# Kernel tuning notes

Hardware: AMD Instinct MI355X
Metric: run time of the kernel (lower is better)

The kernel has to match this reference:

```python
import jax, jax.numpy as jnp
import numpy as np

DIM = 2048
N_HEADS = 16
HEAD_DIM = DIM // N_HEADS
MAX_SEQ_LEN = 2048
THRESHOLD = 0.7
LN_EPS = 1e-5


def _layernorm(x, g, b):
    mu = jnp.mean(x, axis=-1, keepdims=True)
    var = jnp.mean(jnp.square(x - mu), axis=-1, keepdims=True)
    return (x - mu) * jax.lax.rsqrt(var + LN_EPS) * g + b


def _act_quant(x):
    # 8-bit absmax activation quantization (per-tensor), straight-through
    s = 127.0 / jnp.maximum(jnp.max(jnp.abs(x)), 1e-5)
    xq = jnp.clip(jnp.round(x * s), -128.0, 127.0) / s
    return x + jax.lax.stop_gradient(xq - x)


def _ternary_quant(w):
    # W1.58 ternary: zero weights below threshold*mean|w|, scale = mean |w| over survivors
    delta = THRESHOLD * jnp.mean(jnp.abs(w))
    mask = (jnp.abs(w) > delta).astype(w.dtype)
    alpha = jnp.sum(jnp.abs(w) * mask) / jnp.maximum(jnp.sum(mask), 1.0)
    wq = jnp.sign(w) * mask * alpha
    return w + jax.lax.stop_gradient(wq - w)


def _bitlinear(x, w, g, b):
    x = _layernorm(x, g, b)
    xq = _act_quant(x)
    wq = _ternary_quant(w)
    return xq @ wq.T


def _rope_tables():
    inv = 1.0 / (10000.0 ** (np.arange(0, HEAD_DIM, 2, dtype=np.float32) / HEAD_DIM))
    t = np.arange(MAX_SEQ_LEN, dtype=np.float32)
    ang = np.outer(t, inv)  # (max_seq, head_dim/2)
    return jnp.asarray(np.cos(ang)), jnp.asarray(np.sin(ang))


def _apply_rope(x, cos_t, sin_t):
    # Faithful to source: x is (B, H, S, D) and freqs are indexed by x.shape[1] == H
    n = x.shape[1]
    xr = x.reshape(*x.shape[:-1], HEAD_DIM // 2, 2)
    a, b = xr[..., 0], xr[..., 1]
    c = cos_t[:n][None, :, None, :]  # (1, H, 1, D/2)
    s = sin_t[:n][None, :, None, :]
    out = jnp.stack([a * c - b * s, a * s + b * c], axis=-1)
    return out.reshape(x.shape)


def setup_inputs() -> dict:
    key = jax.random.key(0)
    ks = jax.random.split(key, 5)
    std = np.sqrt(2.0 / DIM)
    d = {"x": jax.random.normal(ks[0], (2, MAX_SEQ_LEN, DIM), dtype=jnp.float32)}
    for i, nm in enumerate(["q", "k", "v", "o"]):
        d[f"w_{nm}"] = jax.random.normal(ks[i + 1], (DIM, DIM), dtype=jnp.float32) * std
        d[f"g_{nm}"] = jnp.ones((DIM,), dtype=jnp.float32)
        d[f"b_{nm}"] = jnp.zeros((DIM,), dtype=jnp.float32)
    return d


def reference(x, w_q, g_q, b_q, w_k, g_k, b_k, w_v, g_v, b_v, w_o, g_o, b_o):
    B, S, _ = x.shape
    cos_t, sin_t = _rope_tables()
    scale = HEAD_DIM ** -0.5

    def split_heads(t):
        return t.reshape(B, S, N_HEADS, HEAD_DIM).transpose(0, 2, 1, 3)

    q = split_heads(_bitlinear(x, w_q, g_q, b_q))
    k = split_heads(_bitlinear(x, w_k, g_k, b_k))
    v = split_heads(_bitlinear(x, w_v, g_v, b_v))
    q = _apply_rope(q, cos_t, sin_t)
    k = _apply_rope(k, cos_t, sin_t)
    scores = jnp.einsum("bhsd,bhtd->bhst", q, k) * scale
    attn = jax.nn.softmax(scores, axis=-1)
    out = jnp.einsum("bhst,bhtd->bhsd", attn, v)
    out = out.transpose(0, 2, 1, 3).reshape(B, S, DIM)
    return _bitlinear(out, w_o, g_o, b_o)
```

## Files before the change

### kernel.cpp

```cpp
#include <hip/hip_runtime.h>
#include <math.h>

#define DIM 2048
#define NROWS 4096
#define WN (DIM*DIM)
#define HEADS 16
#define HDIM 128
#define SEQ 2048

typedef __attribute__((ext_vector_type(8))) short short8;
typedef __attribute__((ext_vector_type(8))) _Float16 half8;
typedef __attribute__((ext_vector_type(4))) float floatx4;
typedef __attribute__((ext_vector_type(4))) int intx4;

__device__ __forceinline__ float bf2f(unsigned short u) {
  return __uint_as_float(((unsigned)u) << 16);
}
__device__ __forceinline__ unsigned short f2bf(float f) {
  unsigned x = __float_as_uint(f);
  x += 0x7FFFu + ((x >> 16) & 1u);
  return (unsigned short)(x >> 16);
}
__device__ __forceinline__ unsigned short f2h(float f) {
  _Float16 h = (_Float16)f;
  return __builtin_bit_cast(unsigned short, h);
}
__device__ __forceinline__ float h2f(unsigned short u) {
  _Float16 h = __builtin_bit_cast(_Float16, u);
  return (float)h;
}

__device__ __forceinline__ void gload_lds16(const void* g, void* l) {
  __builtin_amdgcn_global_load_lds(
      (const __attribute__((address_space(1))) unsigned int*)g,
      (__attribute__((address_space(3))) unsigned int*)l, 16, 0, 0);
}

__device__ __forceinline__ float wredSum(float v) {
  #pragma unroll
  for (int o = 1; o < 64; o <<= 1) v += __shfl_xor(v, o);
  return v;
}
__device__ __forceinline__ float wredMax(float v) {
  #pragma unroll
  for (int o = 1; o < 64; o <<= 1) v = fmaxf(v, __shfl_xor(v, o));
  return v;
}

__device__ __forceinline__ float blockReduceSum(float v, float* red) {
  int tid = threadIdx.x;
  red[tid] = v; __syncthreads();
  for (int s = 128; s > 0; s >>= 1) {
    if (tid < s) red[tid] += red[tid + s];
    __syncthreads();
  }
  float r = red[0]; __syncthreads();
  return r;
}

__device__ __forceinline__ const float* pick_w(const float* a, const float* b,
                                               const float* c, const float* d, int i) {
  return i == 0 ? a : i == 1 ? b : i == 2 ? c : d;
}

__global__ __launch_bounds__(256) void w_abs_partial(
    const float* w0, const float* w1, const float* w2, const float* w3, float* part)
{
  const float4* w4 = (const float4*)pick_w(w0, w1, w2, w3, blockIdx.y);
  float s = 0.f;
  for (int i = blockIdx.x * 256 + threadIdx.x; i < WN / 4; i += 1024 * 256) {
    float4 v = w4[i];
    s += fabsf(v.x) + fabsf(v.y) + fabsf(v.z) + fabsf(v.w);
  }
  __shared__ float red[256];
  float t = blockReduceSum(s, red);
  if (threadIdx.x == 0) part[blockIdx.y * 1024 + blockIdx.x] = t;
}

__global__ __launch_bounds__(256) void w_delta_final(const float* part, float* stats)
{
  float s = 0.f;
  for (int i = threadIdx.x; i < 1024; i += 256) s += part[blockIdx.x * 1024 + i];
  __shared__ float red[256];
  float t = blockReduceSum(s, red);
  if (threadIdx.x == 0) stats[blockIdx.x] = 0.7f * (t / (float)WN);
}

__device__ __forceinline__ signed char tq(float v, float delta) {
  if (fabsf(v) > delta) return (v > 0.f) ? (signed char)1 : (signed char)-1;
  return (signed char)0;
}

__global__ __launch_bounds__(256) void w_maskquant(
    const float* w0, const float* w1, const float* w2, const float* w3,
    const float* stats, float* part2, signed char* tern)
{
  int wi = blockIdx.y;
  const float4* w4 = (const float4*)pick_w(w0, w1, w2, w3, wi);
  float delta = stats[wi];
  char4* out = (char4*)(tern + (size_t)wi * WN);
  float s = 0.f, cnt = 0.f;
  for (int i = blockIdx.x * 256 + threadIdx.x; i < WN / 4; i += 1024 * 256) {
    float4 v = w4[i];
    char4 o;
    float a;
    a = fabsf(v.x); if (a > delta) { s += a; cnt += 1.f; } o.x = tq(v.x, delta);
    a = fabsf(v.y); if (a > delta) { s += a; cnt += 1.f; } o.y = tq(v.y, delta);
    a = fabsf(v.z); if (a > delta) { s += a; cnt += 1.f; } o.z = tq(v.z, delta);
    a = fabsf(v.w); if (a > delta) { s += a; cnt += 1.f; } o.w = tq(v.w, delta);
    out[i] = o;
  }
  __shared__ float red[256];
  float ts = blockReduceSum(s, red);
  float tc = blockReduceSum(cnt, red);
  if (threadIdx.x == 0) {
    part2[((size_t)blockIdx.y * 1024 + blockIdx.x) * 2]     = ts;
    part2[((size_t)blockIdx.y * 1024 + blockIdx.x) * 2 + 1] = tc;
  }
}

__global__ __launch_bounds__(256) void w_alpha_final(const float* part2, float* stats)
{
  float s = 0.f, c = 0.f;
  for (int i = threadIdx.x; i < 1024; i += 256) {
    s += part2[((size_t)blockIdx.x * 1024 + i) * 2];
    c += part2[((size_t)blockIdx.x * 1024 + i) * 2 + 1];
  }
  __shared__ float red[256];
  float ts = blockReduceSum(s, red);
  float tc = blockReduceSum(c, red);
  if (threadIdx.x == 0) stats[4 + blockIdx.x] = ts / fmaxf(tc, 1.f);
}

__global__ __launch_bounds__(256) void ln_absmax3(
    const float* __restrict__ x,
    const float* __restrict__ g0, const float* __restrict__ b0,
    const float* __restrict__ g1, const float* __restrict__ b1,
    const float* __restrict__ g2, const float* __restrict__ b2,
    float* __restrict__ pmax)
{
  const int lane = threadIdx.x & 63;
  const int row = blockIdx.x * 4 + (threadIdx.x >> 6);
  const float* xr = x + (size_t)row * DIM;
  float4 a[8];
  float s = 0.f, sq = 0.f;
  #pragma unroll
  for (int j = 0; j < 8; ++j) {
    a[j] = *(const float4*)(xr + j * 256 + lane * 4);
    s  += a[j].x + a[j].y + a[j].z + a[j].w;
    sq += a[j].x*a[j].x + a[j].y*a[j].y + a[j].z*a[j].z + a[j].w*a[j].w;
  }
  s = wredSum(s); sq = wredSum(sq);
  float mu = s * (1.f / DIM);
  float var = sq * (1.f / DIM) - mu * mu;
  float rstd = 1.f / sqrtf(var + 1e-5f);
  const float* gs[3] = {g0, g1, g2};
  const float* bs[3] = {b0, b1, b2};
  #pragma unroll
  for (int p = 0; p < 3; ++p) {
    float m = 0.f;
    #pragma unroll
    for (int j = 0; j < 8; ++j) {
      float4 gg = *(const float4*)(gs[p] + j * 256 + lane * 4);
      float4 bb = *(const float4*)(bs[p] + j * 256 + lane * 4);
      m = fmaxf(m, fabsf((a[j].x - mu) * rstd * gg.x + bb.x));
      m = fmaxf(m, fabsf((a[j].y - mu) * rstd * gg.y + bb.y));
      m = fmaxf(m, fabsf((a[j].z - mu) * rstd * gg.z + bb.z));
      m = fmaxf(m, fabsf((a[j].w - mu) * rstd * gg.w + bb.w));
    }
    m = wredMax(m);
    if (lane == 0) pmax[(size_t)p * NROWS + row] = m;
  }
}

__global__ __launch_bounds__(256) void absmax_final(
    const float* __restrict__ pmax, unsigned* __restrict__ ambits)
{
  const float* src = pmax + (size_t)blockIdx.x * NROWS;
  float m = 0.f;
  for (int i = threadIdx.x; i < NROWS; i += 256) m = fmaxf(m, src[i]);
  m = wredMax(m);
  __shared__ float red[4];
  if ((threadIdx.x & 63) == 0) red[threadIdx.x >> 6] = m;
  __syncthreads();
  if (threadIdx.x == 0)
    ambits[blockIdx.x] = __float_as_uint(fmaxf(fmaxf(red[0], red[1]), fmaxf(red[2], red[3])));
}

__global__ __launch_bounds__(256) void ln_quant3(
    const float* __restrict__ x,
    const float* __restrict__ g0, const float* __restrict__ b0,
    const float* __restrict__ g1, const float* __restrict__ b1,
    const float* __restrict__ g2, const float* __restrict__ b2,
    const unsigned* __restrict__ ambits,
    signed char* __restrict__ xq0, signed char* __restrict__ xq1,
    signed char* __restrict__ xq2)
{
  const int lane = threadIdx.x & 63;
  const int row = blockIdx.x * 4 + (threadIdx.x >> 6);
  const float* xr = x + (size_t)row * DIM;
  float4 a[8];
  float s = 0.f, sq = 0.f;
  #pragma unroll
  for (int j = 0; j < 8; ++j) {
    a[j] = *(const float4*)(xr + j * 256 + lane * 4);
    s  += a[j].x + a[j].y + a[j].z + a[j].w;
    sq += a[j].x*a[j].x + a[j].y*a[j].y + a[j].z*a[j].z + a[j].w*a[j].w;
  }
  s = wredSum(s); sq = wredSum(sq);
  float mu = s * (1.f / DIM);
  float var = sq * (1.f / DIM) - mu * mu;
  float rstd = 1.f / sqrtf(var + 1e-5f);
  const float* gs[3] = {g0, g1, g2};
  const float* bs[3] = {b0, b1, b2};
  signed char* outs[3] = {xq0, xq1, xq2};
  #pragma unroll
  for (int p = 0; p < 3; ++p) {
    float sc = 127.f / fmaxf(__uint_as_float(ambits[p]), 1e-5f);
    #pragma unroll
    for (int j = 0; j < 8; ++j) {
      float4 gg = *(const float4*)(gs[p] + j * 256 + lane * 4);
      float4 bb = *(const float4*)(bs[p] + j * 256 + lane * 4);
      float y0 = (a[j].x - mu) * rstd * gg.x + bb.x;
      float y1 = (a[j].y - mu) * rstd * gg.y + bb.y;
      float y2 = (a[j].z - mu) * rstd * gg.z + bb.z;
      float y3 = (a[j].w - mu) * rstd * gg.w + bb.w;
      char4 q;
      q.x = (signed char)(int)fminf(fmaxf(rintf(y0 * sc), -128.f), 127.f);
      q.y = (signed char)(int)fminf(fmaxf(rintf(y1 * sc), -128.f), 127.f);
      q.z = (signed char)(int)fminf(fmaxf(rintf(y2 * sc), -128.f), 127.f);
      q.w = (signed char)(int)fminf(fmaxf(rintf(y3 * sc), -128.f), 127.f);
      *(char4*)(outs[p] + (size_t)row * DIM + j * 256 + lane * 4) = q;
    }
  }
}

template<int MODE>
__global__ __launch_bounds__(256) void ln_kernel(
    const float* __restrict__ x, const float* __restrict__ g, const float* __restrict__ bias,
    const unsigned* __restrict__ ambits, float* __restrict__ pmax,
    signed char* __restrict__ xq)
{
  const int lane = threadIdx.x & 63;
  const int row = blockIdx.x * 4 + (threadIdx.x >> 6);
  const float* xr = x + (size_t)row * DIM;
  float4 a[8];
  float s = 0.f, sq = 0.f;
  #pragma unroll
  for (int j = 0; j < 8; ++j) {
    a[j] = *(const float4*)(xr + j * 256 + lane * 4);
    s  += a[j].x + a[j].y + a[j].z + a[j].w;
    sq += a[j].x*a[j].x + a[j].y*a[j].y + a[j].z*a[j].z + a[j].w*a[j].w;
  }
  s = wredSum(s); sq = wredSum(sq);
  float mu = s * (1.f / DIM);
  float var = sq * (1.f / DIM) - mu * mu;
  float rstd = 1.f / sqrtf(var + 1e-5f);
  if (MODE == 0) {
    float m = 0.f;
    #pragma unroll
    for (int j = 0; j < 8; ++j) {
      float4 gg = *(const float4*)(g + j * 256 + lane * 4);
      float4 bb = *(const float4*)(bias + j * 256 + lane * 4);
      m = fmaxf(m, fabsf((a[j].x - mu) * rstd * gg.x + bb.x));
      m = fmaxf(m, fabsf((a[j].y - mu) * rstd * gg.y + bb.y));
      m = fmaxf(m, fabsf((a[j].z - mu) * rstd * gg.z + bb.z));
      m = fmaxf(m, fabsf((a[j].w - mu) * rstd * gg.w + bb.w));
    }
    m = wredMax(m);
    if (lane == 0) pmax[row] = m;
  } else {
    float sc = 127.f / fmaxf(__uint_as_float(*ambits), 1e-5f);
    #pragma unroll
    for (int j = 0; j < 8; ++j) {
      float4 gg = *(const float4*)(g + j * 256 + lane * 4);
      float4 bb = *(const float4*)(bias + j * 256 + lane * 4);
      float y0 = (a[j].x - mu) * rstd * gg.x + bb.x;
      float y1 = (a[j].y - mu) * rstd * gg.y + bb.y;
      float y2 = (a[j].z - mu) * rstd * gg.z + bb.z;
      float y3 = (a[j].w - mu) * rstd * gg.w + bb.w;
      char4 q;
      q.x = (signed char)(int)fminf(fmaxf(rintf(y0 * sc), -128.f), 127.f);
      q.y = (signed char)(int)fminf(fmaxf(rintf(y1 * sc), -128.f), 127.f);
      q.z = (signed char)(int)fminf(fmaxf(rintf(y2 * sc), -128.f), 127.f);
      q.w = (signed char)(int)fminf(fmaxf(rintf(y3 * sc), -128.f), 127.f);
      *(char4*)(xq + (size_t)row * DIM + j * 256 + lane * 4) = q;
    }
  }
}

template<int OMODE>
__global__ __launch_bounds__(256) void gemm_bt(
    const signed char* __restrict__ A, const signed char* __restrict__ Bt,
    void* __restrict__ Cp0, const float* __restrict__ stats, int wi)
{
  const int tid = threadIdx.x;
  const int lane = tid & 63;
  const int w = tid >> 6;
  const int wm = w >> 1, wn = w & 1;
  const int quad = lane >> 4, l16 = lane & 15;
  const int bm = blockIdx.x * 128, bn = blockIdx.y * 128;

  __shared__ __align__(16) signed char As[128 * 128];
  __shared__ __align__(16) signed char Bs[128 * 128];

  const int srow_off = lane >> 3;
  const int scol     = (lane & 7) * 16;

  intx4 acc[4][4];
  #pragma unroll
  for (int i = 0; i < 4; ++i)
    #pragma unroll
    for (int j = 0; j < 4; ++j) acc[i][j] = {0, 0, 0, 0};

  for (int k0 = 0; k0 < DIM; k0 += 128) {
    #pragma unroll
    for (int i = 0; i < 4; ++i) {
      int c = i * 4 + w;
      int row = c * 8 + srow_off;
      gload_lds16(A  + (size_t)(bm + row) * DIM + k0 + scol, &As[c * 1024]);
      gload_lds16(Bt + (size_t)(bn + row) * DIM + k0 + scol, &Bs[c * 1024]);
    }
    __syncthreads();
    #pragma unroll
    for (int kc = 0; kc < 2; ++kc) {
      intx4 af[4], bf[4];
      #pragma unroll
      for (int i = 0; i < 4; ++i)
        af[i] = *(const intx4*)&As[(wm * 64 + i * 16 + l16) * 128 + kc * 64 + quad * 16];
      #pragma unroll
      for (int j = 0; j < 4; ++j)
        bf[j] = *(const intx4*)&Bs[(wn * 64 + j * 16 + l16) * 128 + kc * 64 + quad * 16];
      #pragma unroll
      for (int i = 0; i < 4; ++i)
        #pragma unroll
        for (int j = 0; j < 4; ++j)
          acc[i][j] = __builtin_amdgcn_mfma_i32_16x16x64_i8(af[i], bf[j], acc[i][j], 0, 0, 0);
    }
    __syncthreads();
  }

  const unsigned* am = (const unsigned*)(stats + 8);
  float scale = stats[4 + wi] * fmaxf(__uint_as_float(am[wi]), 1e-5f) * (1.f / 127.f);
  #pragma unroll
  for (int i = 0; i < 4; ++i)
    #pragma unroll
    for (int j = 0; j < 4; ++j)
      #pragma unroll
      for (int r = 0; r < 4; ++r) {
        int m = bm + wm * 64 + i * 16 + quad * 4 + r;
        int n = bn + wn * 64 + j * 16 + l16;
        size_t idx = (size_t)m * DIM + n;
        float v = (float)acc[i][j][r] * scale;
        if (OMODE == 0) ((float*)Cp0)[idx] = v;
        else            ((unsigned short*)Cp0)[idx] = f2h(v);
      }
}

__global__ __launch_bounds__(256) void rope_kernel(unsigned short* q, unsigned short* k)
{
  const float SC = 0.12751741769011063f;
  int idx = blockIdx.x * 256 + threadIdx.x;
  int p = idx & 63;
  int h = (idx >> 6) & (HEADS - 1);
  int r = idx >> 10;
  float inv = exp2f((float)p * -0.20762050593046f);
  float ang = (float)h * inv;
  float sn, cs;
  __sincosf(ang, &sn, &cs);
  size_t base = (size_t)r * DIM + h * HDIM + 2 * p;
  {
    float a = h2f(q[base]), b = h2f(q[base + 1]);
    q[base]     = f2h((a * cs - b * sn) * SC);
    q[base + 1] = f2h((a * sn + b * cs) * SC);
  }
  {
    float a = h2f(k[base]), b = h2f(k[base + 1]);
    k[base]     = f2h(a * cs - b * sn);
    k[base + 1] = f2h(a * sn + b * cs);
  }
}

__global__ __launch_bounds__(256) void transpose_v(
    const unsigned short* __restrict__ vin, unsigned short* __restrict__ vout)
{
  __shared__ __align__(16) unsigned short t[64][72];
  const int tid = threadIdx.x;
  const int c0 = blockIdx.x * 64, r0 = blockIdx.y * 64;
  #pragma unroll
  for (int c = 0; c < 2; ++c) {
    int idx = c * 256 + tid;
    int row = idx >> 3, cb = (idx & 7) << 3;
    *(uint4*)&t[row][cb] = *(const uint4*)(vin + (size_t)(r0 + row) * DIM + c0 + cb);
  }
  __syncthreads();
  const int b = r0 >> 11, s0 = r0 & (SEQ - 1);
  const int h = c0 >> 7, d0 = c0 & (HDIM - 1);
  #pragma unroll
  for (int c = 0; c < 2; ++c) {
    int idx = c * 256 + tid;
    int drow = idx >> 3, sb = (idx & 7) << 3;
    union { unsigned short u[8]; uint4 v; } pk;
    #pragma unroll
    for (int j = 0; j < 8; ++j) pk.u[j] = t[sb + j][drow];
    *(uint4*)(vout + (size_t)((b * HEADS + h) * HDIM + d0 + drow) * SEQ + s0 + sb) = pk.v;
  }
}

__global__ __launch_bounds__(256, 4) void flash_attn(
    const unsigned short* __restrict__ qf, const unsigned short* __restrict__ kf,
    const unsigned short* __restrict__ vt, float* __restrict__ o)
{
  const int tid = threadIdx.x;
  const int lane = tid & 63;
  const int w = tid >> 6;
  const int quad = lane >> 4;
  const int l16 = lane & 15;
  const int L = blockIdx.x;
  const int slot = L >> 3;
  const int bh = ((L & 7) << 2) | (slot >> 5);
  const int qt = slot & 31;
  const int b = bh >> 4;
  const int h = bh & 15;

  __shared__ __align__(16) char Ks[64 * 256];
  __shared__ __align__(16) char Vs[128 * 128];
  __shared__ __align__(16) char Ps[4][16 * 128];

  const size_t qbase = ((size_t)(b * SEQ + qt * 64 + w * 16 + l16)) * DIM + h * HDIM;
  short8 qa[4];
  #pragma unroll
  for (int kc = 0; kc < 4; ++kc)
    qa[kc] = *(const short8*)(qf + qbase + kc * 32 + quad * 8);

  float m_q = -INFINITY;
  float l_q = 0.f;
  floatx4 accO[8];
  #pragma unroll
  for (int i = 0; i < 8; ++i) accO[i] = {0.f, 0.f, 0.f, 0.f};

  const char* kg = (const char*)(kf + (size_t)(b * SEQ) * DIM + h * HDIM);
  const char* vg = (const char*)(vt + (size_t)bh * HDIM * SEQ);

  int koff[4], voff[4];
  #pragma unroll
  for (int j = 0; j < 4; ++j) {
    int c = w * 4 + j;
    int rK = c * 4 + (lane >> 4);
    koff[j] = rK * (DIM * 2) + (((lane & 15) * 16) ^ ((rK & 7) << 4));
    int rV = c * 8 + (lane >> 3);
    voff[j] = rV * (SEQ * 2) + (((lane & 7) * 16) ^ ((rV & 7) << 4));
  }

  for (int kt = 0; kt < SEQ / 64; ++kt) {
    __syncthreads();
    const char* kgb = kg + (size_t)kt * 64 * DIM * 2;
    const char* vgb = vg + (size_t)kt * 128;
    #pragma unroll
    for (int j = 0; j < 4; ++j) {
      int c = w * 4 + j;
      gload_lds16(kgb + koff[j], &Ks[c * 1024]);
      gload_lds16(vgb + voff[j], &Vs[c * 1024]);
    }
    asm volatile("s_waitcnt vmcnt(0)" ::: "memory");
    __syncthreads();

    float sreg[4][4];
    __builtin_amdgcn_s_setprio(1);
    #pragma unroll
    for (int jt = 0; jt < 4; ++jt) {
      floatx4 a0 = {0.f, 0.f, 0.f, 0.f};
      #pragma unroll
      for (int kc = 0; kc < 4; ++kc) {
        int kr = jt * 16 + l16;
        short8 kb = *(const short8*)&Ks[(kr * 256 + kc * 64 + quad * 16) ^ ((kr & 7) << 4)];
        a0 = __builtin_amdgcn_mfma_f32_16x16x32_f16(
            __builtin_bit_cast(half8, kb), __builtin_bit_cast(half8, qa[kc]), a0, 0, 0, 0);
      }
      #pragma unroll
      for (int r = 0; r < 4; ++r) sreg[jt][r] = a0[r];
    }
    __builtin_amdgcn_s_setprio(0);

    float mx = sreg[0][0];
    #pragma unroll
    for (int jt = 0; jt < 4; ++jt)
      #pragma unroll
      for (int r = 0; r < 4; ++r) mx = fmaxf(mx, sreg[jt][r]);
    mx = fmaxf(mx, __shfl_xor(mx, 16));
    mx = fmaxf(mx, __shfl_xor(mx, 32));
    int need = !__all(mx <= m_q + 8.f);
    float mnew, alpha;
    if (need) {
      mnew = fmaxf(m_q, mx);
      alpha = exp2f(m_q - mnew);
      m_q = mnew;
    } else {
      mnew = m_q;
      alpha = 1.f;
    }
    float ssum = 0.f;
    #pragma unroll
    for (int jt = 0; jt < 4; ++jt) {
      ushort4 pk;
      float p0 = exp2f(sreg[jt][0] - mnew);
      float p1 = exp2f(sreg[jt][1] - mnew);
      float p2 = exp2f(sreg[jt][2] - mnew);
      float p3 = exp2f(sreg[jt][3] - mnew);
      pk.x = f2h(p0); pk.y = f2h(p1); pk.z = f2h(p2); pk.w = f2h(p3);
      ssum += (p0 + p1) + (p2 + p3);
      *(ushort4*)&Ps[w][(l16 * 128 + jt * 32 + quad * 8) ^ ((l16 & 7) << 4)] = pk;
    }
    ssum += __shfl_xor(ssum, 16);
    ssum += __shfl_xor(ssum, 32);
    l_q = l_q * alpha + ssum;
    if (need) {
      #pragma unroll
      for (int dt = 0; dt < 8; ++dt)
        #pragma unroll
        for (int r = 0; r < 4; ++r) accO[dt][r] *= alpha;
    }

    __builtin_amdgcn_s_setprio(1);
    #pragma unroll
    for (int kc = 0; kc < 2; ++kc) {
      short8 pf = *(const short8*)&Ps[w][(l16 * 128 + kc * 64 + quad * 16) ^ ((l16 & 7) << 4)];
      #pragma unroll
      for (int dt = 0; dt < 8; ++dt) {
        int vr = dt * 16 + l16;
        short8 vf = *(const short8*)&Vs[(vr * 128 + kc * 64 + quad * 16) ^ ((vr & 7) << 4)];
        accO[dt] = __builtin_amdgcn_mfma_f32_16x16x32_f16(
            __builtin_bit_cast(half8, vf), __builtin_bit_cast(half8, pf), accO[dt], 0, 0, 0);
      }
    }
    __builtin_amdgcn_s_setprio(0);
  }

  float invl = 1.0f / l_q;
  const size_t obase = (size_t)(b * SEQ + qt * 64 + w * 16 + l16) * DIM + h * HDIM;
  #pragma unroll
  for (int dt = 0; dt < 8; ++dt) {
    float4 ov;
    ov.x = accO[dt][0] * invl; ov.y = accO[dt][1] * invl;
    ov.z = accO[dt][2] * invl; ov.w = accO[dt][3] * invl;
    *(float4*)(o + obase + dt * 16 + quad * 4) = ov;
  }
}

extern "C" void kernel_launch(void* const* d_in, const int* in_sizes, int n_in,
                              void* d_out, int out_size, void* d_ws, size_t ws_size,
                              hipStream_t stream)
{
  (void)in_sizes; (void)n_in; (void)out_size; (void)ws_size;
  const float* x = (const float*)d_in[0];
  const float* w[4]; const float* g[4]; const float* bb[4];
  for (int i = 0; i < 4; ++i) {
    w[i]  = (const float*)d_in[1 + 3 * i];
    g[i]  = (const float*)d_in[2 + 3 * i];
    bb[i] = (const float*)d_in[3 + 3 * i];
  }

  char* base = (char*)d_ws;
  size_t off = 0;
  auto alloc = [&](size_t bytes) {
    char* p = base + off;
    off += (bytes + 255) & ~(size_t)255;
    return p;
  };
  const size_t ACTH = (size_t)NROWS * DIM * 2;
  const size_t ACT8 = (size_t)NROWS * DIM;
  float* stats          = (float*)alloc(64);
  float* part1          = (float*)alloc(4 * 1024 * sizeof(float));
  float* part2          = (float*)alloc(4 * 1024 * 2 * sizeof(float));
  float* pmax           = (float*)alloc((size_t)4 * NROWS * sizeof(float));
  signed char* tern     = (signed char*)alloc((size_t)4 * WN);
  signed char* xq0      = (signed char*)alloc(ACT8);
  signed char* xq1      = (signed char*)alloc(ACT8);
  signed char* xq2      = (signed char*)alloc(ACT8);
  unsigned short* qh    = (unsigned short*)alloc(ACTH);
  unsigned short* kh    = (unsigned short*)alloc(ACTH);
  unsigned short* vb    = (unsigned short*)alloc(ACTH);
  unsigned short* vtb   = (unsigned short*)alloc(ACTH);
  float* oat            = (float*)alloc((size_t)NROWS * DIM * sizeof(float));
  signed char* xqo = xq0;
  unsigned* ambits = (unsigned*)(stats + 8);

  hipMemsetAsync(stats, 0, 64, stream);

  dim3 b256(256);
  w_abs_partial<<<dim3(1024, 4), b256, 0, stream>>>(w[0], w[1], w[2], w[3], part1);
  w_delta_final<<<4, b256, 0, stream>>>(part1, stats);
  w_maskquant<<<dim3(1024, 4), b256, 0, stream>>>(w[0], w[1], w[2], w[3], stats, part2, tern);
  w_alpha_final<<<4, b256, 0, stream>>>(part2, stats);

  ln_absmax3<<<NROWS / 4, b256, 0, stream>>>(x, g[0], bb[0], g[1], bb[1], g[2], bb[2], pmax);
  absmax_final<<<3, b256, 0, stream>>>(pmax, ambits);
  ln_quant3<<<NROWS / 4, b256, 0, stream>>>(x, g[0], bb[0], g[1], bb[1], g[2], bb[2], ambits,
                                            xq0, xq1, xq2);

  dim3 ggrid(NROWS / 128, DIM / 128);
  gemm_bt<1><<<ggrid, b256, 0, stream>>>(xq0, tern + (size_t)0 * WN, qh, stats, 0);
  gemm_bt<1><<<ggrid, b256, 0, stream>>>(xq1, tern + (size_t)1 * WN, kh, stats, 1);
  gemm_bt<1><<<ggrid, b256, 0, stream>>>(xq2, tern + (size_t)2 * WN, vb, stats, 2);

  rope_kernel<<<NROWS * 1024 / 256, b256, 0, stream>>>(qh, kh);
  transpose_v<<<dim3(DIM / 64, NROWS / 64), b256, 0, stream>>>(vb, vtb);
  flash_attn<<<dim3(32 * 32), b256, 0, stream>>>(qh, kh, vtb, oat);

  ln_kernel<0><<<NROWS / 4, b256, 0, stream>>>(oat, g[3], bb[3], nullptr,
                                               pmax + (size_t)3 * NROWS, nullptr);
  absmax_final<<<1, b256, 0, stream>>>(pmax + (size_t)3 * NROWS, ambits + 3);
  ln_kernel<1><<<NROWS / 4, b256, 0, stream>>>(oat, g[3], bb[3], ambits + 3, nullptr, xqo);
  gemm_bt<0><<<ggrid, b256, 0, stream>>>(xqo, tern + (size_t)3 * WN, (float*)d_out, stats, 3);
}
```

Measured before the change: 461.5 us.

## Batch QKV int8 GEMMs into one launch and fuse V transpose into epilogue

```diff
diff --git a/kernel.cpp b/kernel.cpp
--- a/kernel.cpp
+++ b/kernel.cpp
@@ -13,14 +13,6 @@
 typedef __attribute__((ext_vector_type(4))) float floatx4;
 typedef __attribute__((ext_vector_type(4))) int intx4;
 
-__device__ __forceinline__ float bf2f(unsigned short u) {
-  return __uint_as_float(((unsigned)u) << 16);
-}
-__device__ __forceinline__ unsigned short f2bf(float f) {
-  unsigned x = __float_as_uint(f);
-  x += 0x7FFFu + ((x >> 16) & 1u);
-  return (unsigned short)(x >> 16);
-}
 __device__ __forceinline__ unsigned short f2h(float f) {
   _Float16 h = (_Float16)f;
   return __builtin_bit_cast(unsigned short, h);
@@ -289,10 +281,11 @@
   }
 }
 
-template<int OMODE>
-__global__ __launch_bounds__(256) void gemm_bt(
-    const signed char* __restrict__ A, const signed char* __restrict__ Bt,
-    void* __restrict__ Cp0, const float* __restrict__ stats, int wi)
+__global__ __launch_bounds__(256) void gemm_qkv(
+    const signed char* __restrict__ A0, const signed char* __restrict__ A1,
+    const signed char* __restrict__ A2, const signed char* __restrict__ Bt0,
+    unsigned short* __restrict__ C0, unsigned short* __restrict__ C1,
+    unsigned short* __restrict__ C2t, const float* __restrict__ stats)
 {
   const int tid = threadIdx.x;
   const int lane = tid & 63;
@@ -300,9 +293,14 @@
   const int wm = w >> 1, wn = w & 1;
   const int quad = lane >> 4, l16 = lane & 15;
   const int bm = blockIdx.x * 128, bn = blockIdx.y * 128;
-
-  __shared__ __align__(16) signed char As[128 * 128];
-  __shared__ __align__(16) signed char Bs[128 * 128];
+  const int z = blockIdx.z;
+
+  const signed char* A  = z == 0 ? A0 : z == 1 ? A1 : A2;
+  const signed char* Bt = Bt0 + (size_t)z * WN;
+
+  __shared__ __align__(16) signed char smem[2 * 128 * 128];
+  signed char* As = smem;
+  signed char* Bs = smem + 128 * 128;
 
   const int srow_off = lane >> 3;
   const int scol     = (lane & 7) * 16;
@@ -341,6 +339,98 @@
   }
 
   const unsigned* am = (const unsigned*)(stats + 8);
+  float scale = stats[4 + z] * fmaxf(__uint_as_float(am[z]), 1e-5f) * (1.f / 127.f);
+
+  if (z < 2) {
+    unsigned short* Cp = z == 0 ? C0 : C1;
+    #pragma unroll
+    for (int i = 0; i < 4; ++i)
+      #pragma unroll
+      for (int j = 0; j < 4; ++j)
+        #pragma unroll
+        for (int r = 0; r < 4; ++r) {
+          int m = bm + wm * 64 + i * 16 + quad * 4 + r;
+          int n = bn + wn * 64 + j * 16 + l16;
+          Cp[(size_t)m * DIM + n] = f2h((float)acc[i][j][r] * scale);
+        }
+  } else {
+    #pragma unroll
+    for (int i = 0; i < 4; ++i)
+      #pragma unroll
+      for (int j = 0; j < 4; ++j)
+        #pragma unroll
+        for (int r = 0; r < 4; ++r) {
+          int s = wm * 64 + i * 16 + quad * 4 + r;
+          int d = wn * 64 + j * 16 + l16;
+          int byte = (d * 256 + s * 2) ^ ((d & 7) << 4);
+          *(unsigned short*)(smem + byte) = f2h((float)acc[i][j][r] * scale);
+        }
+    __syncthreads();
+    const int b = bm >> 11;
+    const int s_base = bm & (SEQ - 1);
+    const int h = blockIdx.y;
+    const int sc = (tid & 15) * 8;
+    #pragma unroll
+    for (int pass = 0; pass < 8; ++pass) {
+      int d = (tid >> 4) + pass * 16;
+      int byte = (d * 256 + sc * 2) ^ ((d & 7) << 4);
+      *(uint4*)(C2t + ((size_t)(b * HEADS + h) * HDIM + d) * SEQ + s_base + sc) =
+          *(const uint4*)(smem + byte);
+    }
+  }
+}
+
+__global__ __launch_bounds__(256) void gemm_bt(
+    const signed char* __restrict__ A, const signed char* __restrict__ Bt,
+    float* __restrict__ Cp, const float* __restrict__ stats, int wi)
+{
+  const int tid = threadIdx.x;
+  const int lane = tid & 63;
+  const int w = tid >> 6;
+  const int wm = w >> 1, wn = w & 1;
+  const int quad = lane >> 4, l16 = lane & 15;
+  const int bm = blockIdx.x * 128, bn = blockIdx.y * 128;
+
+  __shared__ __align__(16) signed char As[128 * 128];
+  __shared__ __align__(16) signed char Bs[128 * 128];
+
+  const int srow_off = lane >> 3;
+  const int scol     = (lane & 7) * 16;
+
+  intx4 acc[4][4];
+  #pragma unroll
+  for (int i = 0; i < 4; ++i)
+    #pragma unroll
+    for (int j = 0; j < 4; ++j) acc[i][j] = {0, 0, 0, 0};
+
+  for (int k0 = 0; k0 < DIM; k0 += 128) {
+    #pragma unroll
+    for (int i = 0; i < 4; ++i) {
+      int c = i * 4 + w;
+      int row = c * 8 + srow_off;
+      gload_lds16(A  + (size_t)(bm + row) * DIM + k0 + scol, &As[c * 1024]);
+      gload_lds16(Bt + (size_t)(bn + row) * DIM + k0 + scol, &Bs[c * 1024]);
+    }
+    __syncthreads();
+    #pragma unroll
+    for (int kc = 0; kc < 2; ++kc) {
+      intx4 af[4], bf[4];
+      #pragma unroll
+      for (int i = 0; i < 4; ++i)
+        af[i] = *(const intx4*)&As[(wm * 64 + i * 16 + l16) * 128 + kc * 64 + quad * 16];
+      #pragma unroll
+      for (int j = 0; j < 4; ++j)
+        bf[j] = *(const intx4*)&Bs[(wn * 64 + j * 16 + l16) * 128 + kc * 64 + quad * 16];
+      #pragma unroll
+      for (int i = 0; i < 4; ++i)
+        #pragma unroll
+        for (int j = 0; j < 4; ++j)
+          acc[i][j] = __builtin_amdgcn_mfma_i32_16x16x64_i8(af[i], bf[j], acc[i][j], 0, 0, 0);
+    }
+    __syncthreads();
+  }
+
+  const unsigned* am = (const unsigned*)(stats + 8);
   float scale = stats[4 + wi] * fmaxf(__uint_as_float(am[wi]), 1e-5f) * (1.f / 127.f);
   #pragma unroll
   for (int i = 0; i < 4; ++i)
@@ -350,10 +440,7 @@
       for (int r = 0; r < 4; ++r) {
         int m = bm + wm * 64 + i * 16 + quad * 4 + r;
         int n = bn + wn * 64 + j * 16 + l16;
-        size_t idx = (size_t)m * DIM + n;
-        float v = (float)acc[i][j][r] * scale;
-        if (OMODE == 0) ((float*)Cp0)[idx] = v;
-        else            ((unsigned short*)Cp0)[idx] = f2h(v);
+        Cp[(size_t)m * DIM + n] = (float)acc[i][j][r] * scale;
       }
 }
 
@@ -378,32 +465,6 @@
     float a = h2f(k[base]), b = h2f(k[base + 1]);
     k[base]     = f2h(a * cs - b * sn);
     k[base + 1] = f2h(a * sn + b * cs);
-  }
-}
-
-__global__ __launch_bounds__(256) void transpose_v(
-    const unsigned short* __restrict__ vin, unsigned short* __restrict__ vout)
-{
-  __shared__ __align__(16) unsigned short t[64][72];
-  const int tid = threadIdx.x;
-  const int c0 = blockIdx.x * 64, r0 = blockIdx.y * 64;
-  #pragma unroll
-  for (int c = 0; c < 2; ++c) {
-    int idx = c * 256 + tid;
-    int row = idx >> 3, cb = (idx & 7) << 3;
-    *(uint4*)&t[row][cb] = *(const uint4*)(vin + (size_t)(r0 + row) * DIM + c0 + cb);
-  }
-  __syncthreads();
-  const int b = r0 >> 11, s0 = r0 & (SEQ - 1);
-  const int h = c0 >> 7, d0 = c0 & (HDIM - 1);
-  #pragma unroll
-  for (int c = 0; c < 2; ++c) {
-    int idx = c * 256 + tid;
-    int drow = idx >> 3, sb = (idx & 7) << 3;
-    union { unsigned short u[8]; uint4 v; } pk;
-    #pragma unroll
-    for (int j = 0; j < 8; ++j) pk.u[j] = t[sb + j][drow];
-    *(uint4*)(vout + (size_t)((b * HEADS + h) * HDIM + d0 + drow) * SEQ + s0 + sb) = pk.v;
   }
 }
 
@@ -579,7 +640,6 @@
   signed char* xq2      = (signed char*)alloc(ACT8);
   unsigned short* qh    = (unsigned short*)alloc(ACTH);
   unsigned short* kh    = (unsigned short*)alloc(ACTH);
-  unsigned short* vb    = (unsigned short*)alloc(ACTH);
   unsigned short* vtb   = (unsigned short*)alloc(ACTH);
   float* oat            = (float*)alloc((size_t)NROWS * DIM * sizeof(float));
   signed char* xqo = xq0;
@@ -598,18 +658,16 @@
   ln_quant3<<<NROWS / 4, b256, 0, stream>>>(x, g[0], bb[0], g[1], bb[1], g[2], bb[2], ambits,
                                             xq0, xq1, xq2);
 
-  dim3 ggrid(NROWS / 128, DIM / 128);
-  gemm_bt<1><<<ggrid, b256, 0, stream>>>(xq0, tern + (size_t)0 * WN, qh, stats, 0);
-  gemm_bt<1><<<ggrid, b256, 0, stream>>>(xq1, tern + (size_t)1 * WN, kh, stats, 1);
-  gemm_bt<1><<<ggrid, b256, 0, stream>>>(xq2, tern + (size_t)2 * WN, vb, stats, 2);
+  gemm_qkv<<<dim3(NROWS / 128, DIM / 128, 3), b256, 0, stream>>>(
+      xq0, xq1, xq2, tern, qh, kh, vtb, stats);
 
   rope_kernel<<<NROWS * 1024 / 256, b256, 0, stream>>>(qh, kh);
-  transpose_v<<<dim3(DIM / 64, NROWS / 64), b256, 0, stream>>>(vb, vtb);
   flash_attn<<<dim3(32 * 32), b256, 0, stream>>>(qh, kh, vtb, oat);
 
   ln_kernel<0><<<NROWS / 4, b256, 0, stream>>>(oat, g[3], bb[3], nullptr,
                                                pmax + (size_t)3 * NROWS, nullptr);
   absmax_final<<<1, b256, 0, stream>>>(pmax + (size_t)3 * NROWS, ambits + 3);
   ln_kernel<1><<<NROWS / 4, b256, 0, stream>>>(oat, g[3], bb[3], ambits + 3, nullptr, xqo);
-  gemm_bt<0><<<ggrid, b256, 0, stream>>>(xqo, tern + (size_t)3 * WN, (float*)d_out, stats, 3);
-}
+  gemm_bt<<<dim3(NROWS / 128, DIM / 128), b256, 0, stream>>>(
+      xqo, tern + (size_t)3 * WN, (float*)d_out, stats, 3);
+}
```

Result: faster. 442.6 us (-4.1%).
